# Performance work log

Hardware: AMD Instinct MI355X
Metric: run time of the kernel (lower is better)

The kernel has to match this reference:

```python
import jax, jax.numpy as jnp
import numpy as np

N = 10000   # total nodes
I = 1000    # input nodes   [0, I)
F = 8600    # function nodes [I, I+F)
O = 400     # output nodes  [I+F, N)
E = 80000   # edges
C = 16      # channels per function node
LAYERS = 6
B = 64
EPS = 1e-5  # torch LayerNorm default eps


def _build_graph():
    rng = np.random.default_rng(0)
    fn = np.arange(I, I + F)
    out = np.arange(I + F, N)
    n_if, n_fo = 10000, O
    n_ff = E - n_if - n_fo
    # input -> function (every input node appears as src at least once)
    src_if = np.concatenate([np.arange(I), rng.integers(0, I, n_if - I)])
    dst_if = rng.integers(I, I + F, n_if)
    # function -> function (every function node appears as dst at least once)
    src_ff = rng.integers(I, I + F, n_ff)
    dst_ff = np.concatenate([fn, rng.integers(I, I + F, n_ff - F)])
    # function -> output (each output node has exactly one incoming edge)
    src_fo = rng.integers(I, I + F, n_fo)
    dst_fo = out
    src = np.concatenate([src_if, src_ff, src_fo]).astype(np.int32)
    dst = np.concatenate([dst_if, dst_ff, dst_fo]).astype(np.int32)
    return src, dst


def setup_inputs() -> dict:
    key = jax.random.key(0)
    ks = jax.random.split(key, 8)
    src, dst = _build_graph()
    fn_idx = np.arange(I, I + F).astype(np.int32)
    input_edge_mask = (src < I).astype(np.float32)   # edges leaving input nodes
    fn_src_mask = (src >= I).astype(np.float32)      # W3 only has entries for function-node sources
    last_edge = np.zeros(N, dtype=np.int32)
    has = np.zeros(N, dtype=np.float32)
    last_edge[dst] = np.arange(E)
    has[dst] = 1.0
    s = 1.0 / np.sqrt(C)
    return dict(
        x=jax.random.normal(ks[0], (B, N), jnp.float32),
        w1=jax.random.normal(ks[1], (E, C), jnp.float32) * s,            # lin1 nnz: (e, dst(e)*C+c)
        b1=jax.random.normal(ks[2], (N, C), jnp.float32) * 0.01,
        w2=jax.random.normal(ks[3], (F, C, C), jnp.float32) * s,         # lin2: dense CxC per function node
        b2=jax.random.normal(ks[4], (N, C), jnp.float32) * 0.01,
        w3=jax.random.normal(ks[5], (E, C), jnp.float32) * s * fn_src_mask[:, None],  # lin3 nnz: (src(e)*C+c, e)
        b3=jax.random.normal(ks[6], (E,), jnp.float32) * 0.01,
        scale_out=jnp.ones((1, E, 1), jnp.float32),
        bias_out=jnp.zeros((1, E, 1), jnp.float32),
        src=jnp.asarray(src), dst=jnp.asarray(dst), fn_idx=jnp.asarray(fn_idx),
        input_edge_mask=jnp.asarray(input_edge_mask),
        last_edge=jnp.asarray(last_edge), has_edge=jnp.asarray(has),
    )


def _forward(x, w1, b1, w2, b2, w3, b3, scale_out, bias_out,
             src, dst, fn_idx, input_edge_mask, last_edge, has_edge):
    x0 = x[:, src]                                   # node2edge gather: (B, E)
    xe = x0
    m = input_edge_mask[None, :]                     # (1, E)
    for _ in range(LAYERS):                          # eval mode: full depth, no dropout
        x_last = xe
        # lin1 (sparse E -> C*N): scatter-add edge contributions into dst-node channels
        h = jnp.zeros((B, N, C), x.dtype).at[:, dst, :].add(xe[:, :, None] * w1[None])
        h = jax.nn.elu(h + b1)
        # lin2 (block-diagonal CxC over function nodes); other node channels get bias only
        hf = jnp.einsum('bfc,fcd->bfd', h[:, fn_idx], w2)
        h2 = jax.nn.elu(jnp.zeros((B, N, C), x.dtype).at[:, fn_idx, :].set(hf) + b2)
        # lin3 (sparse C*N -> E): gather src-node channels per edge, contract over C
        xe = jnp.einsum('bec,ec->be', h2[:, src], w3) + b3
        xe = xe + x_last                             # residual
        mu = jnp.mean(xe, axis=-1, keepdims=True)    # LayerNorm over E, no affine
        var = jnp.mean((xe - mu) ** 2, axis=-1, keepdims=True)
        xn = (xe - mu) * jax.lax.rsqrt(var + EPS)
        xe = (1.0 - m) * xn + m * x0                 # pin input edges to x0
    xe = scale_out[0, :, 0][None, :] * xe + bias_out[0, :, 0][None, :]
    return xe[:, last_edge] * has_edge[None, :]      # (B, N)


def reference(x, w1, b1, w2, b2, w3, b3, scale_out, bias_out,
              src, dst, fn_idx, input_edge_mask, last_edge, has_edge):
    return _forward(x, w1, b1, w2, b2, w3, b3, scale_out, bias_out,
                    src, dst, fn_idx, input_edge_mask, last_edge, has_edge)
```

## Files before the change

### kernel.cpp

```cpp
#include <hip/hip_runtime.h>
#include <math.h>

#define NN 10000
#define NI 1000
#define NF 8600
#define NE 80000
#define NC 16
#define NB 64
#define NS (NI + NF)
#define NLAYERS 6
#define LN_EPS 1e-5f
#define PF 8

#define LAYER_BLOCKS ((NS + 7) / 8)
#define TILE_BLOCKS ((NN + 63) / 64)

typedef float f32x4 __attribute__((ext_vector_type(4)));

__device__ __forceinline__ float elu_fast(float x) {
    return x > 0.0f ? x : __expf(x) - 1.0f;
}

__global__ __launch_bounds__(256) void k_transpose(const float* __restrict__ x,
                                                   float* __restrict__ xT) {
    __shared__ float t[64][65];
    int n0 = blockIdx.x * 64;
    int lane = threadIdx.x & 63, w = threadIdx.x >> 6;
    int n = n0 + lane;
    for (int bb = w; bb < 64; bb += 4)
        t[bb][lane] = (n < NN) ? x[(size_t)bb * NN + n] : 0.f;
    __syncthreads();
    for (int nn = w; nn < 64; nn += 4) {
        int nw = n0 + nn;
        if (nw < NN) xT[(size_t)nw * 64 + lane] = t[lane][nn];
    }
}

__global__ void k_count(const int* __restrict__ src, const int* __restrict__ dst,
                        int* __restrict__ cs, int* __restrict__ cd) {
    int e = blockIdx.x * blockDim.x + threadIdx.x;
    if (e >= NE) return;
    atomicAdd(&cs[src[e]], 1);
    int d = dst[e];
    if (d >= NI && d < NI + NF) atomicAdd(&cd[d - NI], 1);
}

__global__ void k_scan(const int* __restrict__ cnt, int* __restrict__ rp, int L) {
    __shared__ int tsum[1024];
    int t = threadIdx.x;
    int per = (L + 1023) >> 10;
    int beg = t * per;
    int end = beg + per; if (end > L) end = L;
    int s = 0;
    for (int i = beg; i < end; ++i) s += cnt[i];
    tsum[t] = s;
    __syncthreads();
    for (int off = 1; off < 1024; off <<= 1) {
        int v = (t >= off) ? tsum[t - off] : 0;
        __syncthreads();
        tsum[t] += v;
        __syncthreads();
    }
    int run = (t == 0) ? 0 : tsum[t - 1];
    for (int i = beg; i < end; ++i) { rp[i] = run; run += cnt[i]; }
    if (t == 1023) rp[L] = tsum[1023];
}

__global__ void k_copyoff(const int* __restrict__ rp_s, const int* __restrict__ rp_d,
                          int* __restrict__ off_s, int* __restrict__ off_d,
                          int* __restrict__ foCtr) {
    int i = blockIdx.x * blockDim.x + threadIdx.x;
    if (i < NS) off_s[i] = rp_s[i];
    if (i < NF) off_d[i] = rp_d[i];
    if (i == 0) foCtr[0] = rp_d[NF];
}

__global__ void k_fill(const int* __restrict__ src, const int* __restrict__ dst,
                       int* __restrict__ off_s, int* __restrict__ off_d,
                       int* __restrict__ foCtr,
                       int* __restrict__ el_s, int* __restrict__ el_d,
                       int* __restrict__ posOf) {
    int e = blockIdx.x * blockDim.x + threadIdx.x;
    if (e >= NE) return;
    int p = atomicAdd(&off_s[src[e]], 1);
    el_s[p] = e;
    int d = dst[e];
    int q;
    if (d >= NI && d < NI + NF) {
        q = atomicAdd(&off_d[d - NI], 1);
        el_d[q] = e;
    } else {
        q = atomicAdd(foCtr, 1);
    }
    posOf[e] = q;
}

__global__ void k_permute(const int* __restrict__ src,
                          const float* __restrict__ w1, const float* __restrict__ w3,
                          const float* __restrict__ b3, const float* __restrict__ b2,
                          const int* __restrict__ rp_d,
                          const int* __restrict__ el_d, const int* __restrict__ el_s,
                          const int* __restrict__ posOf,
                          unsigned* __restrict__ pd, unsigned* __restrict__ pe2,
                          float* __restrict__ w1g, float* __restrict__ w3g,
                          float* __restrict__ b3g, float* __restrict__ c3) {
    int k = blockIdx.x * blockDim.x + threadIdx.x;
    if (k >= NE) return;
    {
        int e = el_s[k];
        int s = src[e];
        pe2[k] = (unsigned)(posOf[e] * NB);
        float wrow[NC];
        const f32x4* s4 = (const f32x4*)(w3 + (size_t)e * NC);
        ((f32x4*)wrow)[0] = s4[0]; ((f32x4*)wrow)[1] = s4[1];
        ((f32x4*)wrow)[2] = s4[2]; ((f32x4*)wrow)[3] = s4[3];
        f32x4* d4 = (f32x4*)(w3g + (size_t)k * NC);
        d4[0] = ((f32x4*)wrow)[0]; d4[1] = ((f32x4*)wrow)[1];
        d4[2] = ((f32x4*)wrow)[2]; d4[3] = ((f32x4*)wrow)[3];
        float bb = b3[e];
        b3g[k] = bb;
        float cc = 0.f;
        if (s < NI) {
            const float* b2r = b2 + (size_t)s * NC;
            #pragma unroll
            for (int c = 0; c < NC; ++c) {
                float h = b2r[c];
                h = h > 0.f ? h : __expf(h) - 1.0f;
                cc += h * wrow[c];
            }
            cc += bb;
        }
        c3[k] = cc;
    }
    if (k < rp_d[NF]) {
        int e = el_d[k];
        int s = src[e];
        unsigned off = (s < NI) ? (unsigned)(s * NB) : (unsigned)(k * NB);
        pd[k] = (off << 1) | (s < NI ? 0u : 1u);
        const f32x4* s4 = (const f32x4*)(w1 + (size_t)e * NC);
        f32x4* d4 = (f32x4*)(w1g + (size_t)k * NC);
        d4[0] = s4[0]; d4[1] = s4[1]; d4[2] = s4[2]; d4[3] = s4[3];
    }
}

__global__ void k_init_xe(const float* __restrict__ xT, const int* __restrict__ src,
                          const int* __restrict__ posOf,
                          float* __restrict__ xeA, float* __restrict__ accum) {
    size_t idx = (size_t)blockIdx.x * blockDim.x + threadIdx.x;
    if (idx < (NLAYERS + 1) * 128) {
        float v = 0.f;
        if (idx >= 64 && idx < 128) v = (float)NE * (1.0f - LN_EPS);
        accum[idx] = v;
    }
    if (idx >= (size_t)NE * NB) return;
    int e = (int)(idx >> 6), b = (int)(idx & 63);
    xeA[(size_t)posOf[e] * NB + b] = xT[(size_t)src[e] * NB + b];
}

__global__ __launch_bounds__(512, 4) void k_layer(
    const float* __restrict__ xT,
    const float* __restrict__ xeR, float* __restrict__ xeW,
    const float* __restrict__ sums, float* __restrict__ sumsOut,
    const float* __restrict__ w1g, const float* __restrict__ b1,
    const float* __restrict__ w2, const float* __restrict__ b2,
    const float* __restrict__ w3g, const float* __restrict__ b3g,
    const float* __restrict__ c3,
    const int* __restrict__ rp_d, const unsigned* __restrict__ pd,
    const int* __restrict__ rp_s, const unsigned* __restrict__ pe2)
{
    __shared__ float shs[512], shq[512];
    int lane = threadIdx.x & 63;
    int s = __builtin_amdgcn_readfirstlane((int)(blockIdx.x * 8 + (threadIdx.x >> 6)));
    float lsum = 0.f, lsq = 0.f;
    if (s < NS) {
        int k0s = __builtin_amdgcn_readfirstlane(rp_s[s]);
        int k1s = __builtin_amdgcn_readfirstlane(rp_s[s + 1]);
        if (s < NI) {
            float x0v = xT[(size_t)s * NB + lane];
            for (int k = k0s; k < k1s; ++k) {
                float v = x0v + c3[k];
                lsum += v; lsq += v * v;
            }
        } else {
            const float inv = 1.0f / (float)NE;
            float mu = sums[lane] * inv;
            float rs = rsqrtf(sums[64 + lane] * inv - mu * mu + LN_EPS);
            int f = s - NI;

            float acc[NC];
            {
                const f32x4* b1r = (const f32x4*)(b1 + (size_t)s * NC);
                f32x4 a = b1r[0], b = b1r[1], c = b1r[2], d = b1r[3];
                acc[0]=a.x; acc[1]=a.y; acc[2]=a.z; acc[3]=a.w;
                acc[4]=b.x; acc[5]=b.y; acc[6]=b.z; acc[7]=b.w;
                acc[8]=c.x; acc[9]=c.y; acc[10]=c.z; acc[11]=c.w;
                acc[12]=d.x; acc[13]=d.y; acc[14]=d.z; acc[15]=d.w;
            }
            int k0d = __builtin_amdgcn_readfirstlane(rp_d[f]);
            int k1d = __builtin_amdgcn_readfirstlane(rp_d[f + 1]);
            for (int base = k0d; base < k1d; base += PF) {
                int m = k1d - base; if (m > PF) m = PF;
                unsigned pv[PF];
                #pragma unroll
                for (int j = 0; j < PF; ++j) pv[j] = (j < m) ? pd[base + j] : 0u;
                float raw[PF];
                #pragma unroll
                for (int j = 0; j < PF; ++j)
                    if (j < m) {
                        const float* bp = (pv[j] & 1u) ? xeR : xT;
                        raw[j] = bp[(size_t)(pv[j] >> 1) + lane];
                    }
                #pragma unroll
                for (int j = 0; j < PF; ++j) {
                    if (j < m) {
                        float xv = (pv[j] & 1u) ? (raw[j] - mu) * rs : raw[j];
                        const f32x4* wr = (const f32x4*)(w1g + (size_t)(base + j) * NC);
                        f32x4 a = wr[0], b = wr[1], c = wr[2], d = wr[3];
                        acc[0]  += xv * a.x; acc[1]  += xv * a.y; acc[2]  += xv * a.z; acc[3]  += xv * a.w;
                        acc[4]  += xv * b.x; acc[5]  += xv * b.y; acc[6]  += xv * b.z; acc[7]  += xv * b.w;
                        acc[8]  += xv * c.x; acc[9]  += xv * c.y; acc[10] += xv * c.z; acc[11] += xv * c.w;
                        acc[12] += xv * d.x; acc[13] += xv * d.y; acc[14] += xv * d.z; acc[15] += xv * d.w;
                    }
                }
            }

            float h[NC];
            #pragma unroll
            for (int c = 0; c < NC; ++c) h[c] = elu_fast(acc[c]);

            float hf[NC];
            {
                const f32x4* b2r = (const f32x4*)(b2 + (size_t)s * NC);
                f32x4 a = b2r[0], b = b2r[1], c = b2r[2], d = b2r[3];
                hf[0]=a.x; hf[1]=a.y; hf[2]=a.z; hf[3]=a.w;
                hf[4]=b.x; hf[5]=b.y; hf[6]=b.z; hf[7]=b.w;
                hf[8]=c.x; hf[9]=c.y; hf[10]=c.z; hf[11]=c.w;
                hf[12]=d.x; hf[13]=d.y; hf[14]=d.z; hf[15]=d.w;
            }
            const float* w2f = w2 + (size_t)f * NC * NC;
            #pragma unroll
            for (int c = 0; c < NC; ++c) {
                const f32x4* w2r = (const f32x4*)(w2f + c * NC);
                f32x4 a = w2r[0], b = w2r[1], cc = w2r[2], d = w2r[3];
                float hc = h[c];
                hf[0]  += hc * a.x;  hf[1]  += hc * a.y;  hf[2]  += hc * a.z;  hf[3]  += hc * a.w;
                hf[4]  += hc * b.x;  hf[5]  += hc * b.y;  hf[6]  += hc * b.z;  hf[7]  += hc * b.w;
                hf[8]  += hc * cc.x; hf[9]  += hc * cc.y; hf[10] += hc * cc.z; hf[11] += hc * cc.w;
                hf[12] += hc * d.x;  hf[13] += hc * d.y;  hf[14] += hc * d.z;  hf[15] += hc * d.w;
            }
            float hv[NC];
            #pragma unroll
            for (int c = 0; c < NC; ++c) hv[c] = elu_fast(hf[c]);

            for (int base = k0s; base < k1s; base += PF) {
                int m = k1s - base; if (m > PF) m = PF;
                unsigned pos[PF];
                #pragma unroll
                for (int j = 0; j < PF; ++j) pos[j] = (j < m) ? pe2[base + j] : 0u;
                float old[PF];
                #pragma unroll
                for (int j = 0; j < PF; ++j)
                    if (j < m) old[j] = xeR[(size_t)pos[j] + lane];
                #pragma unroll
                for (int j = 0; j < PF; ++j) {
                    if (j < m) {
                        float xl = (old[j] - mu) * rs;
                        const f32x4* wr = (const f32x4*)(w3g + (size_t)(base + j) * NC);
                        f32x4 a = wr[0], b = wr[1], c = wr[2], d = wr[3];
                        float v = b3g[base + j] + xl;
                        v += hv[0]*a.x + hv[1]*a.y + hv[2]*a.z + hv[3]*a.w;
                        v += hv[4]*b.x + hv[5]*b.y + hv[6]*b.z + hv[7]*b.w;
                        v += hv[8]*c.x + hv[9]*c.y + hv[10]*c.z + hv[11]*c.w;
                        v += hv[12]*d.x + hv[13]*d.y + hv[14]*d.z + hv[15]*d.w;
                        xeW[(size_t)pos[j] + lane] = v;
                        lsum += v; lsq += v * v;
                    }
                }
            }
        }
    }
    shs[threadIdx.x] = lsum; shq[threadIdx.x] = lsq;
    __syncthreads();
    int t = threadIdx.x;
    if (t < 64) {
        float ts = 0.f;
        #pragma unroll
        for (int w = 0; w < 8; ++w) ts += shs[w * 64 + t];
        atomicAdd(&sumsOut[t], ts);
    } else if (t < 128) {
        int l = t - 64;
        float tq = 0.f;
        #pragma unroll
        for (int w = 0; w < 8; ++w) tq += shq[w * 64 + l];
        atomicAdd(&sumsOut[64 + l], tq);
    }
}

__global__ __launch_bounds__(256) void k_out(
    const float* __restrict__ xT, const float* __restrict__ xeF,
    const float* __restrict__ sums,
    const int* __restrict__ src, const int* __restrict__ posOf,
    const float* __restrict__ scale, const float* __restrict__ bias,
    const int* __restrict__ last_edge, const float* __restrict__ has,
    float* __restrict__ out)
{
    __shared__ float t[64][65];
    int n0 = blockIdx.x * 64;
    int lane = threadIdx.x & 63, w = threadIdx.x >> 6;
    const float inv = 1.0f / (float)NE;
    float mu = sums[lane] * inv;
    float rs = rsqrtf(sums[64 + lane] * inv - mu * mu + LN_EPS);
    for (int nn = w; nn < 64; nn += 4) {
        int n = n0 + nn;
        float val = 0.f;
        if (n < NN) {
            int le = last_edge[n];
            int s = src[le];
            float x0v = xT[(size_t)s * NB + lane];
            float xn = (xeF[(size_t)posOf[le] * NB + lane] - mu) * rs;
            float xf = (s < NI) ? x0v : xn;
            val = has[n] * (scale[le] * xf + bias[le]);
        }
        t[nn][lane] = val;
    }
    __syncthreads();
    for (int bb = w; bb < 64; bb += 4) {
        int n = n0 + lane;
        if (n < NN) out[(size_t)bb * NN + n] = t[lane][bb];
    }
}

extern "C" void kernel_launch(void* const* d_in, const int* in_sizes, int n_in,
                              void* d_out, int out_size, void* d_ws, size_t ws_size,
                              hipStream_t stream) {
    const float* x     = (const float*)d_in[0];
    const float* w1    = (const float*)d_in[1];
    const float* b1    = (const float*)d_in[2];
    const float* w2    = (const float*)d_in[3];
    const float* b2    = (const float*)d_in[4];
    const float* w3    = (const float*)d_in[5];
    const float* b3    = (const float*)d_in[6];
    const float* scale = (const float*)d_in[7];
    const float* bias  = (const float*)d_in[8];
    const int*   src   = (const int*)d_in[9];
    const int*   dst   = (const int*)d_in[10];
    const int*   last  = (const int*)d_in[13];
    const float* has   = (const float*)d_in[14];
    float* out = (float*)d_out;

    char* p = (char*)d_ws;
    auto alloc = [&](size_t bytes) {
        char* r = p;
        p += (bytes + 255) & ~(size_t)255;
        return r;
    };
    float* xT    = (float*)alloc((size_t)NN * NB * 4);
    float* xeA   = (float*)alloc((size_t)NE * NB * 4);
    float* xeB   = (float*)alloc((size_t)NE * NB * 4);
    float* accum = (float*)alloc((NLAYERS + 1) * 128 * 4);
    float* w1g   = (float*)alloc((size_t)NE * NC * 4);
    float* w3g   = (float*)alloc((size_t)NE * NC * 4);
    float* b3g   = (float*)alloc((size_t)NE * 4);
    float* c3    = (float*)alloc((size_t)NE * 4);
    unsigned* pd  = (unsigned*)alloc((size_t)NE * 4);
    unsigned* pe2 = (unsigned*)alloc((size_t)NE * 4);
    int* rp_s  = (int*)alloc((NS + 1) * 4);
    int* rp_d  = (int*)alloc((NF + 1) * 4);
    int* el_s  = (int*)alloc((size_t)NE * 4);
    int* el_d  = (int*)alloc((size_t)NE * 4);
    int* posOf = (int*)alloc((size_t)NE * 4);
    int* off_s = (int*)alloc(NS * 4);
    int* off_d = (int*)alloc(NF * 4);
    int* cs    = (int*)alloc(NS * 4);
    int* cd    = (int*)alloc(NF * 4);
    int* foCtr = (int*)alloc(4);

    hipMemsetAsync(cs, 0, NS * 4, stream);
    hipMemsetAsync(cd, 0, NF * 4, stream);
    k_transpose<<<TILE_BLOCKS, 256, 0, stream>>>(x, xT);
    k_count<<<(NE + 255) / 256, 256, 0, stream>>>(src, dst, cs, cd);
    k_scan<<<1, 1024, 0, stream>>>(cs, rp_s, NS);
    k_scan<<<1, 1024, 0, stream>>>(cd, rp_d, NF);
    k_copyoff<<<(NS + 255) / 256, 256, 0, stream>>>(rp_s, rp_d, off_s, off_d, foCtr);
    k_fill<<<(NE + 255) / 256, 256, 0, stream>>>(src, dst, off_s, off_d, foCtr,
                                                 el_s, el_d, posOf);
    k_permute<<<(NE + 255) / 256, 256, 0, stream>>>(src, w1, w3, b3, b2, rp_d,
                                                    el_d, el_s, posOf,
                                                    pd, pe2, w1g, w3g, b3g, c3);
    k_init_xe<<<(int)(((size_t)NE * NB + 255) / 256), 256, 0, stream>>>(xT, src, posOf,
                                                                        xeA, accum);

    for (int L = 0; L < NLAYERS; ++L) {
        const float* xeR = (L & 1) ? xeB : xeA;
        float*       xeW = (L & 1) ? xeA : xeB;
        k_layer<<<LAYER_BLOCKS, 512, 0, stream>>>(xT, xeR, xeW,
                                                  accum + L * 128, accum + (L + 1) * 128,
                                                  w1g, b1, w2, b2, w3g, b3g, c3,
                                                  rp_d, pd, rp_s, pe2);
    }
    k_out<<<TILE_BLOCKS, 256, 0, stream>>>(xT, xeA, accum + NLAYERS * 128, src, posOf,
                                           scale, bias, last, has, out);
}
```

Before: 378.5 us.

## Store edge states in source-sorted order and hoist constant input-edge stats

Edge activations are now stored in source-node order, so each function node writes its outgoing edges contiguously. This removes the pe2 indirection on the store path, and pd is remapped so the gather side still finds its inputs. Input-edge contributions to the LayerNorm sums do not change across layers, so they are computed once by a new kernel and pre-added into every layer's accumulator; the layer kernel then covers only function nodes with 256-thread blocks. The two scans are merged into one launch and the first xe load is prefetched ahead of the lin2 math. Gathers on the destination side stay irregular.

```diff
diff --git a/kernel.cpp b/kernel.cpp
--- a/kernel.cpp
+++ b/kernel.cpp
@@ -12,7 +12,7 @@
 #define LN_EPS 1e-5f
 #define PF 8
 
-#define LAYER_BLOCKS ((NS + 7) / 8)
+#define LAYER_BLOCKS ((NF + 3) / 4)
 #define TILE_BLOCKS ((NN + 63) / 64)
 
 typedef float f32x4 __attribute__((ext_vector_type(4)));
@@ -45,8 +45,12 @@
     if (d >= NI && d < NI + NF) atomicAdd(&cd[d - NI], 1);
 }
 
-__global__ void k_scan(const int* __restrict__ cnt, int* __restrict__ rp, int L) {
+__global__ void k_scan2(const int* __restrict__ cs, const int* __restrict__ cd,
+                        int* __restrict__ rps, int* __restrict__ rpd) {
     __shared__ int tsum[1024];
+    const int* cnt; int* rp; int L;
+    if (blockIdx.x == 0) { cnt = cs; rp = rps; L = NS; }
+    else                 { cnt = cd; rp = rpd; L = NF; }
     int t = threadIdx.x;
     int per = (L + 1023) >> 10;
     int beg = t * per;
@@ -67,32 +71,26 @@
 }
 
 __global__ void k_copyoff(const int* __restrict__ rp_s, const int* __restrict__ rp_d,
-                          int* __restrict__ off_s, int* __restrict__ off_d,
-                          int* __restrict__ foCtr) {
+                          int* __restrict__ off_s, int* __restrict__ off_d) {
     int i = blockIdx.x * blockDim.x + threadIdx.x;
     if (i < NS) off_s[i] = rp_s[i];
     if (i < NF) off_d[i] = rp_d[i];
-    if (i == 0) foCtr[0] = rp_d[NF];
 }
 
 __global__ void k_fill(const int* __restrict__ src, const int* __restrict__ dst,
                        int* __restrict__ off_s, int* __restrict__ off_d,
-                       int* __restrict__ foCtr,
                        int* __restrict__ el_s, int* __restrict__ el_d,
-                       int* __restrict__ posOf) {
+                       int* __restrict__ posOfS) {
     int e = blockIdx.x * blockDim.x + threadIdx.x;
     if (e >= NE) return;
     int p = atomicAdd(&off_s[src[e]], 1);
     el_s[p] = e;
+    posOfS[e] = p;
     int d = dst[e];
-    int q;
     if (d >= NI && d < NI + NF) {
-        q = atomicAdd(&off_d[d - NI], 1);
+        int q = atomicAdd(&off_d[d - NI], 1);
         el_d[q] = e;
-    } else {
-        q = atomicAdd(foCtr, 1);
-    }
-    posOf[e] = q;
+    }
 }
 
 __global__ void k_permute(const int* __restrict__ src,
@@ -100,16 +98,17 @@
                           const float* __restrict__ b3, const float* __restrict__ b2,
                           const int* __restrict__ rp_d,
                           const int* __restrict__ el_d, const int* __restrict__ el_s,
-                          const int* __restrict__ posOf,
-                          unsigned* __restrict__ pd, unsigned* __restrict__ pe2,
+                          const int* __restrict__ posOfS,
+                          unsigned* __restrict__ pd,
                           float* __restrict__ w1g, float* __restrict__ w3g,
-                          float* __restrict__ b3g, float* __restrict__ c3) {
+                          float* __restrict__ b3g, float* __restrict__ c3,
+                          int* __restrict__ srcS) {
     int k = blockIdx.x * blockDim.x + threadIdx.x;
     if (k >= NE) return;
     {
         int e = el_s[k];
         int s = src[e];
-        pe2[k] = (unsigned)(posOf[e] * NB);
+        srcS[k] = s;
         float wrow[NC];
         const f32x4* s4 = (const f32x4*)(w3 + (size_t)e * NC);
         ((f32x4*)wrow)[0] = s4[0]; ((f32x4*)wrow)[1] = s4[1];
@@ -135,7 +134,7 @@
     if (k < rp_d[NF]) {
         int e = el_d[k];
         int s = src[e];
-        unsigned off = (s < NI) ? (unsigned)(s * NB) : (unsigned)(k * NB);
+        unsigned off = (s < NI) ? (unsigned)(s * NB) : (unsigned)(posOfS[e] * NB);
         pd[k] = (off << 1) | (s < NI ? 0u : 1u);
         const f32x4* s4 = (const f32x4*)(w1 + (size_t)e * NC);
         f32x4* d4 = (f32x4*)(w1g + (size_t)k * NC);
@@ -143,8 +142,7 @@
     }
 }
 
-__global__ void k_init_xe(const float* __restrict__ xT, const int* __restrict__ src,
-                          const int* __restrict__ posOf,
+__global__ void k_init_xe(const float* __restrict__ xT, const int* __restrict__ srcS,
                           float* __restrict__ xeA, float* __restrict__ accum) {
     size_t idx = (size_t)blockIdx.x * blockDim.x + threadIdx.x;
     if (idx < (NLAYERS + 1) * 128) {
@@ -153,128 +151,153 @@
         accum[idx] = v;
     }
     if (idx >= (size_t)NE * NB) return;
-    int e = (int)(idx >> 6), b = (int)(idx & 63);
-    xeA[(size_t)posOf[e] * NB + b] = xT[(size_t)src[e] * NB + b];
-}
-
-__global__ __launch_bounds__(512, 4) void k_layer(
+    int k = (int)(idx >> 6), b = (int)(idx & 63);
+    xeA[idx] = xT[(size_t)srcS[k] * NB + b];
+}
+
+__global__ __launch_bounds__(256) void k_cstats(
+    const float* __restrict__ xT, const int* __restrict__ srcS,
+    const float* __restrict__ c3, const int* __restrict__ rp_s,
+    float* __restrict__ accum)
+{
+    __shared__ float shs[256], shq[256];
+    int lane = threadIdx.x & 63;
+    int nIn = __builtin_amdgcn_readfirstlane(rp_s[NI]);
+    float ls = 0.f, lq = 0.f;
+    for (int k = blockIdx.x * 4 + (threadIdx.x >> 6); k < nIn; k += gridDim.x * 4) {
+        float v = xT[(size_t)srcS[k] * NB + lane] + c3[k];
+        ls += v; lq += v * v;
+    }
+    shs[threadIdx.x] = ls; shq[threadIdx.x] = lq;
+    __syncthreads();
+    int t = threadIdx.x;
+    if (t < 64) {
+        float ts = shs[t] + shs[64 + t] + shs[128 + t] + shs[192 + t];
+        #pragma unroll
+        for (int L = 1; L <= NLAYERS; ++L) atomicAdd(&accum[L * 128 + t], ts);
+    } else if (t < 128) {
+        int l = t - 64;
+        float tq = shq[l] + shq[64 + l] + shq[128 + l] + shq[192 + l];
+        #pragma unroll
+        for (int L = 1; L <= NLAYERS; ++L) atomicAdd(&accum[L * 128 + 64 + l], tq);
+    }
+}
+
+__global__ __launch_bounds__(256, 6) void k_layer(
     const float* __restrict__ xT,
     const float* __restrict__ xeR, float* __restrict__ xeW,
     const float* __restrict__ sums, float* __restrict__ sumsOut,
     const float* __restrict__ w1g, const float* __restrict__ b1,
     const float* __restrict__ w2, const float* __restrict__ b2,
     const float* __restrict__ w3g, const float* __restrict__ b3g,
-    const float* __restrict__ c3,
     const int* __restrict__ rp_d, const unsigned* __restrict__ pd,
-    const int* __restrict__ rp_s, const unsigned* __restrict__ pe2)
+    const int* __restrict__ rp_s)
 {
-    __shared__ float shs[512], shq[512];
+    __shared__ float shs[256], shq[256];
     int lane = threadIdx.x & 63;
-    int s = __builtin_amdgcn_readfirstlane((int)(blockIdx.x * 8 + (threadIdx.x >> 6)));
+    int f = __builtin_amdgcn_readfirstlane((int)(blockIdx.x * 4 + (threadIdx.x >> 6)));
     float lsum = 0.f, lsq = 0.f;
-    if (s < NS) {
-        int k0s = __builtin_amdgcn_readfirstlane(rp_s[s]);
-        int k1s = __builtin_amdgcn_readfirstlane(rp_s[s + 1]);
-        if (s < NI) {
-            float x0v = xT[(size_t)s * NB + lane];
-            for (int k = k0s; k < k1s; ++k) {
-                float v = x0v + c3[k];
-                lsum += v; lsq += v * v;
+    if (f < NF) {
+        int n = NI + f;
+        const float inv = 1.0f / (float)NE;
+        float mu = sums[lane] * inv;
+        float rs = rsqrtf(sums[64 + lane] * inv - mu * mu + LN_EPS);
+
+        float acc[NC];
+        {
+            const f32x4* b1r = (const f32x4*)(b1 + (size_t)n * NC);
+            f32x4 a = b1r[0], b = b1r[1], c = b1r[2], d = b1r[3];
+            acc[0]=a.x; acc[1]=a.y; acc[2]=a.z; acc[3]=a.w;
+            acc[4]=b.x; acc[5]=b.y; acc[6]=b.z; acc[7]=b.w;
+            acc[8]=c.x; acc[9]=c.y; acc[10]=c.z; acc[11]=c.w;
+            acc[12]=d.x; acc[13]=d.y; acc[14]=d.z; acc[15]=d.w;
+        }
+        int k0d = __builtin_amdgcn_readfirstlane(rp_d[f]);
+        int k1d = __builtin_amdgcn_readfirstlane(rp_d[f + 1]);
+        for (int base = k0d; base < k1d; base += PF) {
+            int m = k1d - base; if (m > PF) m = PF;
+            unsigned pv[PF];
+            #pragma unroll
+            for (int j = 0; j < PF; ++j) pv[j] = (j < m) ? pd[base + j] : 0u;
+            float raw[PF];
+            #pragma unroll
+            for (int j = 0; j < PF; ++j)
+                if (j < m) {
+                    const float* bp = (pv[j] & 1u) ? xeR : xT;
+                    raw[j] = bp[(size_t)(pv[j] >> 1) + lane];
+                }
+            #pragma unroll
+            for (int j = 0; j < PF; ++j) {
+                if (j < m) {
+                    float xv = (pv[j] & 1u) ? (raw[j] - mu) * rs : raw[j];
+                    const f32x4* wr = (const f32x4*)(w1g + (size_t)(base + j) * NC);
+                    f32x4 a = wr[0], b = wr[1], c = wr[2], d = wr[3];
+                    acc[0]  += xv * a.x; acc[1]  += xv * a.y; acc[2]  += xv * a.z; acc[3]  += xv * a.w;
+                    acc[4]  += xv * b.x; acc[5]  += xv * b.y; acc[6]  += xv * b.z; acc[7]  += xv * b.w;
+                    acc[8]  += xv * c.x; acc[9]  += xv * c.y; acc[10] += xv * c.z; acc[11] += xv * c.w;
+                    acc[12] += xv * d.x; acc[13] += xv * d.y; acc[14] += xv * d.z; acc[15] += xv * d.w;
+                }
             }
-        } else {
-            const float inv = 1.0f / (float)NE;
-            float mu = sums[lane] * inv;
-            float rs = rsqrtf(sums[64 + lane] * inv - mu * mu + LN_EPS);
-            int f = s - NI;
-
-            float acc[NC];
-            {
-                const f32x4* b1r = (const f32x4*)(b1 + (size_t)s * NC);
-                f32x4 a = b1r[0], b = b1r[1], c = b1r[2], d = b1r[3];
-                acc[0]=a.x; acc[1]=a.y; acc[2]=a.z; acc[3]=a.w;
-                acc[4]=b.x; acc[5]=b.y; acc[6]=b.z; acc[7]=b.w;
-                acc[8]=c.x; acc[9]=c.y; acc[10]=c.z; acc[11]=c.w;
-                acc[12]=d.x; acc[13]=d.y; acc[14]=d.z; acc[15]=d.w;
-            }
-            int k0d = __builtin_amdgcn_readfirstlane(rp_d[f]);
-            int k1d = __builtin_amdgcn_readfirstlane(rp_d[f + 1]);
-            for (int base = k0d; base < k1d; base += PF) {
-                int m = k1d - base; if (m > PF) m = PF;
-                unsigned pv[PF];
+        }
+
+        int k0s = __builtin_amdgcn_readfirstlane(rp_s[n]);
+        int k1s = __builtin_amdgcn_readfirstlane(rp_s[n + 1]);
+        int m0 = k1s - k0s; if (m0 > PF) m0 = PF;
+        float old0[PF];
+        #pragma unroll
+        for (int j = 0; j < PF; ++j)
+            if (j < m0) old0[j] = xeR[(size_t)(k0s + j) * NB + lane];
+
+        float h[NC];
+        #pragma unroll
+        for (int c = 0; c < NC; ++c) h[c] = elu_fast(acc[c]);
+        float hf[NC];
+        {
+            const f32x4* b2r = (const f32x4*)(b2 + (size_t)n * NC);
+            f32x4 a = b2r[0], b = b2r[1], c = b2r[2], d = b2r[3];
+            hf[0]=a.x; hf[1]=a.y; hf[2]=a.z; hf[3]=a.w;
+            hf[4]=b.x; hf[5]=b.y; hf[6]=b.z; hf[7]=b.w;
+            hf[8]=c.x; hf[9]=c.y; hf[10]=c.z; hf[11]=c.w;
+            hf[12]=d.x; hf[13]=d.y; hf[14]=d.z; hf[15]=d.w;
+        }
+        const float* w2f = w2 + (size_t)f * NC * NC;
+        #pragma unroll
+        for (int c = 0; c < NC; ++c) {
+            const f32x4* w2r = (const f32x4*)(w2f + c * NC);
+            f32x4 a = w2r[0], b = w2r[1], cc = w2r[2], d = w2r[3];
+            float hc = h[c];
+            hf[0]  += hc * a.x;  hf[1]  += hc * a.y;  hf[2]  += hc * a.z;  hf[3]  += hc * a.w;
+            hf[4]  += hc * b.x;  hf[5]  += hc * b.y;  hf[6]  += hc * b.z;  hf[7]  += hc * b.w;
+            hf[8]  += hc * cc.x; hf[9]  += hc * cc.y; hf[10] += hc * cc.z; hf[11] += hc * cc.w;
+            hf[12] += hc * d.x;  hf[13] += hc * d.y;  hf[14] += hc * d.z;  hf[15] += hc * d.w;
+        }
+        float hv[NC];
+        #pragma unroll
+        for (int c = 0; c < NC; ++c) hv[c] = elu_fast(hf[c]);
+
+        for (int base = k0s; base < k1s; base += PF) {
+            int m = k1s - base; if (m > PF) m = PF;
+            float old[PF];
+            if (base == k0s) {
                 #pragma unroll
-                for (int j = 0; j < PF; ++j) pv[j] = (j < m) ? pd[base + j] : 0u;
-                float raw[PF];
+                for (int j = 0; j < PF; ++j) old[j] = old0[j];
+            } else {
                 #pragma unroll
                 for (int j = 0; j < PF; ++j)
-                    if (j < m) {
-                        const float* bp = (pv[j] & 1u) ? xeR : xT;
-                        raw[j] = bp[(size_t)(pv[j] >> 1) + lane];
-                    }
-                #pragma unroll
-                for (int j = 0; j < PF; ++j) {
-                    if (j < m) {
-                        float xv = (pv[j] & 1u) ? (raw[j] - mu) * rs : raw[j];
-                        const f32x4* wr = (const f32x4*)(w1g + (size_t)(base + j) * NC);
-                        f32x4 a = wr[0], b = wr[1], c = wr[2], d = wr[3];
-                        acc[0]  += xv * a.x; acc[1]  += xv * a.y; acc[2]  += xv * a.z; acc[3]  += xv * a.w;
-                        acc[4]  += xv * b.x; acc[5]  += xv * b.y; acc[6]  += xv * b.z; acc[7]  += xv * b.w;
-                        acc[8]  += xv * c.x; acc[9]  += xv * c.y; acc[10] += xv * c.z; acc[11] += xv * c.w;
-                        acc[12] += xv * d.x; acc[13] += xv * d.y; acc[14] += xv * d.z; acc[15] += xv * d.w;
-                    }
-                }
+                    if (j < m) old[j] = xeR[(size_t)(base + j) * NB + lane];
             }
-
-            float h[NC];
             #pragma unroll
-            for (int c = 0; c < NC; ++c) h[c] = elu_fast(acc[c]);
-
-            float hf[NC];
-            {
-                const f32x4* b2r = (const f32x4*)(b2 + (size_t)s * NC);
-                f32x4 a = b2r[0], b = b2r[1], c = b2r[2], d = b2r[3];
-                hf[0]=a.x; hf[1]=a.y; hf[2]=a.z; hf[3]=a.w;
-                hf[4]=b.x; hf[5]=b.y; hf[6]=b.z; hf[7]=b.w;
-                hf[8]=c.x; hf[9]=c.y; hf[10]=c.z; hf[11]=c.w;
-                hf[12]=d.x; hf[13]=d.y; hf[14]=d.z; hf[15]=d.w;
-            }
-            const float* w2f = w2 + (size_t)f * NC * NC;
-            #pragma unroll
-            for (int c = 0; c < NC; ++c) {
-                const f32x4* w2r = (const f32x4*)(w2f + c * NC);
-                f32x4 a = w2r[0], b = w2r[1], cc = w2r[2], d = w2r[3];
-                float hc = h[c];
-                hf[0]  += hc * a.x;  hf[1]  += hc * a.y;  hf[2]  += hc * a.z;  hf[3]  += hc * a.w;
-                hf[4]  += hc * b.x;  hf[5]  += hc * b.y;  hf[6]  += hc * b.z;  hf[7]  += hc * b.w;
-                hf[8]  += hc * cc.x; hf[9]  += hc * cc.y; hf[10] += hc * cc.z; hf[11] += hc * cc.w;
-                hf[12] += hc * d.x;  hf[13] += hc * d.y;  hf[14] += hc * d.z;  hf[15] += hc * d.w;
-            }
-            float hv[NC];
-            #pragma unroll
-            for (int c = 0; c < NC; ++c) hv[c] = elu_fast(hf[c]);
-
-            for (int base = k0s; base < k1s; base += PF) {
-                int m = k1s - base; if (m > PF) m = PF;
-                unsigned pos[PF];
-                #pragma unroll
-                for (int j = 0; j < PF; ++j) pos[j] = (j < m) ? pe2[base + j] : 0u;
-                float old[PF];
-                #pragma unroll
-                for (int j = 0; j < PF; ++j)
-                    if (j < m) old[j] = xeR[(size_t)pos[j] + lane];
-                #pragma unroll
-                for (int j = 0; j < PF; ++j) {
-                    if (j < m) {
-                        float xl = (old[j] - mu) * rs;
-                        const f32x4* wr = (const f32x4*)(w3g + (size_t)(base + j) * NC);
-                        f32x4 a = wr[0], b = wr[1], c = wr[2], d = wr[3];
-                        float v = b3g[base + j] + xl;
-                        v += hv[0]*a.x + hv[1]*a.y + hv[2]*a.z + hv[3]*a.w;
-                        v += hv[4]*b.x + hv[5]*b.y + hv[6]*b.z + hv[7]*b.w;
-                        v += hv[8]*c.x + hv[9]*c.y + hv[10]*c.z + hv[11]*c.w;
-                        v += hv[12]*d.x + hv[13]*d.y + hv[14]*d.z + hv[15]*d.w;
-                        xeW[(size_t)pos[j] + lane] = v;
-                        lsum += v; lsq += v * v;
-                    }
+            for (int j = 0; j < PF; ++j) {
+                if (j < m) {
+                    const f32x4* wr = (const f32x4*)(w3g + (size_t)(base + j) * NC);
+                    f32x4 a = wr[0], b = wr[1], c = wr[2], d = wr[3];
+                    float v = b3g[base + j] + (old[j] - mu) * rs;
+                    v += hv[0]*a.x + hv[1]*a.y + hv[2]*a.z + hv[3]*a.w;
+                    v += hv[4]*b.x + hv[5]*b.y + hv[6]*b.z + hv[7]*b.w;
+                    v += hv[8]*c.x + hv[9]*c.y + hv[10]*c.z + hv[11]*c.w;
+                    v += hv[12]*d.x + hv[13]*d.y + hv[14]*d.z + hv[15]*d.w;
+                    xeW[(size_t)(base + j) * NB + lane] = v;
+                    lsum += v; lsq += v * v;
                 }
             }
         }
@@ -283,15 +306,11 @@
     __syncthreads();
     int t = threadIdx.x;
     if (t < 64) {
-        float ts = 0.f;
-        #pragma unroll
-        for (int w = 0; w < 8; ++w) ts += shs[w * 64 + t];
+        float ts = shs[t] + shs[64 + t] + shs[128 + t] + shs[192 + t];
         atomicAdd(&sumsOut[t], ts);
     } else if (t < 128) {
         int l = t - 64;
-        float tq = 0.f;
-        #pragma unroll
-        for (int w = 0; w < 8; ++w) tq += shq[w * 64 + l];
+        float tq = shq[l] + shq[64 + l] + shq[128 + l] + shq[192 + l];
         atomicAdd(&sumsOut[64 + l], tq);
     }
 }
@@ -299,7 +318,7 @@
 __global__ __launch_bounds__(256) void k_out(
     const float* __restrict__ xT, const float* __restrict__ xeF,
     const float* __restrict__ sums,
-    const int* __restrict__ src, const int* __restrict__ posOf,
+    const int* __restrict__ src, const int* __restrict__ posOfS,
     const float* __restrict__ scale, const float* __restrict__ bias,
     const int* __restrict__ last_edge, const float* __restrict__ has,
     float* __restrict__ out)
@@ -317,7 +336,7 @@
             int le = last_edge[n];
             int s = src[le];
             float x0v = xT[(size_t)s * NB + lane];
-            float xn = (xeF[(size_t)posOf[le] * NB + lane] - mu) * rs;
+            float xn = (xeF[(size_t)posOfS[le] * NB + lane] - mu) * rs;
             float xf = (s < NI) ? x0v : xn;
             val = has[n] * (scale[le] * xf + bias[le]);
         }
@@ -362,42 +381,41 @@
     float* w3g   = (float*)alloc((size_t)NE * NC * 4);
     float* b3g   = (float*)alloc((size_t)NE * 4);
     float* c3    = (float*)alloc((size_t)NE * 4);
-    unsigned* pd  = (unsigned*)alloc((size_t)NE * 4);
-    unsigned* pe2 = (unsigned*)alloc((size_t)NE * 4);
-    int* rp_s  = (int*)alloc((NS + 1) * 4);
-    int* rp_d  = (int*)alloc((NF + 1) * 4);
-    int* el_s  = (int*)alloc((size_t)NE * 4);
-    int* el_d  = (int*)alloc((size_t)NE * 4);
-    int* posOf = (int*)alloc((size_t)NE * 4);
-    int* off_s = (int*)alloc(NS * 4);
-    int* off_d = (int*)alloc(NF * 4);
-    int* cs    = (int*)alloc(NS * 4);
-    int* cd    = (int*)alloc(NF * 4);
-    int* foCtr = (int*)alloc(4);
+    unsigned* pd = (unsigned*)alloc((size_t)NE * 4);
+    int* rp_s   = (int*)alloc((NS + 1) * 4);
+    int* rp_d   = (int*)alloc((NF + 1) * 4);
+    int* el_s   = (int*)alloc((size_t)NE * 4);
+    int* el_d   = (int*)alloc((size_t)NE * 4);
+    int* posOfS = (int*)alloc((size_t)NE * 4);
+    int* srcS   = (int*)alloc((size_t)NE * 4);
+    int* off_s  = (int*)alloc(NS * 4);
+    int* off_d  = (int*)alloc(NF * 4);
+    int* cs     = (int*)alloc(NS * 4);
+    int* cd     = (int*)alloc(NF * 4);
 
     hipMemsetAsync(cs, 0, NS * 4, stream);
     hipMemsetAsync(cd, 0, NF * 4, stream);
     k_transpose<<<TILE_BLOCKS, 256, 0, stream>>>(x, xT);
     k_count<<<(NE + 255) / 256, 256, 0, stream>>>(src, dst, cs, cd);
-    k_scan<<<1, 1024, 0, stream>>>(cs, rp_s, NS);
-    k_scan<<<1, 1024, 0, stream>>>(cd, rp_d, NF);
-    k_copyoff<<<(NS + 255) / 256, 256, 0, stream>>>(rp_s, rp_d, off_s, off_d, foCtr);
-    k_fill<<<(NE + 255) / 256, 256, 0, stream>>>(src, dst, off_s, off_d, foCtr,
-                                                 el_s, el_d, posOf);
+    k_scan2<<<2, 1024, 0, stream>>>(cs, cd, rp_s, rp_d);
+    k_copyoff<<<(NS + 255) / 256, 256, 0, stream>>>(rp_s, rp_d, off_s, off_d);
+    k_fill<<<(NE + 255) / 256, 256, 0, stream>>>(src, dst, off_s, off_d,
+                                                 el_s, el_d, posOfS);
     k_permute<<<(NE + 255) / 256, 256, 0, stream>>>(src, w1, w3, b3, b2, rp_d,
-                                                    el_d, el_s, posOf,
-                                                    pd, pe2, w1g, w3g, b3g, c3);
-    k_init_xe<<<(int)(((size_t)NE * NB + 255) / 256), 256, 0, stream>>>(xT, src, posOf,
+                                                    el_d, el_s, posOfS,
+                                                    pd, w1g, w3g, b3g, c3, srcS);
+    k_init_xe<<<(int)(((size_t)NE * NB + 255) / 256), 256, 0, stream>>>(xT, srcS,
                                                                         xeA, accum);
+    k_cstats<<<128, 256, 0, stream>>>(xT, srcS, c3, rp_s, accum);
 
     for (int L = 0; L < NLAYERS; ++L) {
         const float* xeR = (L & 1) ? xeB : xeA;
         float*       xeW = (L & 1) ? xeA : xeB;
-        k_layer<<<LAYER_BLOCKS, 512, 0, stream>>>(xT, xeR, xeW,
+        k_layer<<<LAYER_BLOCKS, 256, 0, stream>>>(xT, xeR, xeW,
                                                   accum + L * 128, accum + (L + 1) * 128,
-                                                  w1g, b1, w2, b2, w3g, b3g, c3,
-                                                  rp_d, pd, rp_s, pe2);
-    }
-    k_out<<<TILE_BLOCKS, 256, 0, stream>>>(xT, xeA, accum + NLAYERS * 128, src, posOf,
+                                                  w1g, b1, w2, b2, w3g, b3g,
+                                                  rp_d, pd, rp_s);
+    }
+    k_out<<<TILE_BLOCKS, 256, 0, stream>>>(xT, xeA, accum + NLAYERS * 128, src, posOfS,
                                            scale, bias, last, has, out);
 }
```

Result: slower. 520.9 us (+37.6%).
